# Kernel tuning notes

Hardware: AMD Instinct MI355X
Metric: run time of the kernel (lower is better)

## Reference

```python
import jax, jax.numpy as jnp
import numpy as np

N_NODES = 50000
N_EDGES = 800000
D_IN = 96
D_OUT = 96


def setup_inputs() -> dict:
    key = jax.random.key(0)
    k1, k2, k3 = jax.random.split(key, 3)
    x = jax.random.normal(k1, (N_NODES, D_IN), dtype=jnp.float32)
    edge_index = jax.random.randint(k2, (2, N_EDGES), 0, N_NODES, dtype=jnp.int64)
    edge_weight = jnp.ones((N_EDGES,), dtype=jnp.float32)
    # Glorot-ish init for the linear weight, zero bias (as in PyG GCNConv)
    W = jax.random.normal(k3, (D_IN, D_OUT), dtype=jnp.float32) * (1.0 / np.sqrt(D_IN))
    b = jnp.zeros((D_OUT,), dtype=jnp.float32)
    return {"x": x, "edge_index": edge_index, "edge_weight": edge_weight, "W": W, "b": b}


def reference(x, edge_index, edge_weight, W, b):
    """PyG GCNConv: out = D^{-1/2} (A + I) D^{-1/2} (x @ W) + b."""
    N = x.shape[0]
    row, col = edge_index[0], edge_index[1]  # source -> target
    # add self loops with weight 1 (PyG default add_self_loops=True)
    loop = jnp.arange(N, dtype=edge_index.dtype)
    row = jnp.concatenate([row, loop])
    col = jnp.concatenate([col, loop])
    ew = jnp.concatenate([edge_weight, jnp.ones((N,), dtype=edge_weight.dtype)])
    # symmetric normalization based on (weighted) in-degree over col
    deg = jax.ops.segment_sum(ew, col, num_segments=N)  # [N]
    dinv = jnp.where(deg > 0, jax.lax.rsqrt(deg), 0.0)
    norm = dinv[row] * ew * dinv[col]  # [E+N]
    # linear transform first (small GEMM), then gather-scale-scatter over edges
    h = x @ W  # [N, D_OUT]
    msg = h[row] * norm[:, None]  # [E+N, D_OUT]
    out = jax.ops.segment_sum(msg, col, num_segments=N)  # [N, D_OUT]
    return out + b
```

## Files before the change

### kernel.cpp

```cpp
#include <hip/hip_runtime.h>

#define N_NODES 50000
#define N_EDGES 800000
#define D 96
#define NBKT 512
#define BNODES 98
#define BCAP 2304
#define PART_B 250
#define EPB 3200
#define EPT 13
#define CAP 48
#define NSLOT (BNODES * CAP)
#define GCAP 768
#define GEMM_B 782

typedef float vfloat4 __attribute__((ext_vector_type(4)));

__device__ __forceinline__ float bf_lo(unsigned u) { return __uint_as_float(u << 16); }
__device__ __forceinline__ float bf_hi(unsigned u) { return __uint_as_float(u & 0xFFFF0000u); }
__device__ __forceinline__ unsigned f2bf_bits(unsigned u) {
    return (u + 0x7FFFu + ((u >> 16) & 1u)) & 0xFFFF0000u;
}
__device__ __forceinline__ unsigned pack_bf2(float a, float b) {
    return (f2bf_bits(__float_as_uint(a)) >> 16) | f2bf_bits(__float_as_uint(b));
}

__device__ __forceinline__ int exscan256(int v, int* wsum) {
    int lane = threadIdx.x & 63;
    int wave = threadIdx.x >> 6;
    int incl = v;
#pragma unroll
    for (int off = 1; off < 64; off <<= 1) {
        int t = __shfl_up(incl, off);
        if (lane >= off) incl += t;
    }
    if (lane == 63) wsum[wave] = incl;
    __syncthreads();
    int base = 0;
#pragma unroll
    for (int wv = 0; wv < 3; ++wv) base += (wv < wave) ? wsum[wv] : 0;
    return base + incl - v;
}

__global__ __launch_bounds__(256) void k_partgemm(
    const int* __restrict__ row, const int* __restrict__ col,
    const float* __restrict__ ew, const float* __restrict__ x,
    const float* __restrict__ W, int* __restrict__ bkt_cnt,
    uint2* __restrict__ bktbuf, unsigned short* __restrict__ hb) {
    __shared__ int sh[2 * NBKT];
    int tid = threadIdx.x;
    int bid = blockIdx.x;

    if (bid < PART_B) {
        int* hist = sh;
        int* cur = sh + NBKT;
        hist[tid] = 0;
        hist[tid + 256] = 0;
        __syncthreads();
        int e0 = bid * EPB;
        int myc[EPT];
#pragma unroll
        for (int k = 0; k < EPT; ++k) {
            int i = tid + 256 * k;
            myc[k] = (i < EPB) ? col[e0 + i] : -1;
        }
#pragma unroll
        for (int k = 0; k < EPT; ++k)
            if (myc[k] >= 0) atomicAdd(&hist[myc[k] / BNODES], 1);
        __syncthreads();
        {
            int h0 = hist[tid], h1 = hist[tid + 256];
            cur[tid] = h0 ? atomicAdd(&bkt_cnt[tid], h0) : 0;
            cur[tid + 256] = h1 ? atomicAdd(&bkt_cnt[tid + 256], h1) : 0;
        }
        __syncthreads();
#pragma unroll
        for (int k = 0; k < EPT; ++k) {
            int i = tid + 256 * k;
            if (myc[k] >= 0) {
                int e = e0 + i;
                int c = myc[k];
                int b = c / BNODES;
                int p = atomicAdd(&cur[b], 1);
                if (p < BCAP)
                    bktbuf[(size_t)b * BCAP + p] =
                        make_uint2((unsigned)row[e] | ((unsigned)(c - b * BNODES) << 16),
                                   __float_as_uint(ew[e]));
            }
        }
    } else {
        int g = bid - PART_B;
        int lane = tid & 63;
        int j0 = __builtin_amdgcn_readfirstlane((tid >> 6) * 24);
        int n = g * 64 + lane;
        bool act = (n < N_NODES);
        const float* xr = x + (size_t)(act ? n : 0) * D;

        float acc[24] = {};
        for (int k4 = 0; k4 < D / 4; ++k4) {
            float4 xv = *(const float4*)&xr[k4 * 4];
#pragma unroll
            for (int kk = 0; kk < 4; ++kk) {
                float xs = (kk == 0) ? xv.x : (kk == 1) ? xv.y
                         : (kk == 2) ? xv.z : xv.w;
                const float* Wr = W + (k4 * 4 + kk) * D + j0;
#pragma unroll
                for (int jj = 0; jj < 24; ++jj)
                    acc[jj] += xs * Wr[jj];
            }
        }
        if (act) {
            unsigned short* hp = hb + (size_t)n * D + j0;
            uint4 u0, u1, u2;
            u0.x = pack_bf2(acc[0], acc[1]);   u0.y = pack_bf2(acc[2], acc[3]);
            u0.z = pack_bf2(acc[4], acc[5]);   u0.w = pack_bf2(acc[6], acc[7]);
            u1.x = pack_bf2(acc[8], acc[9]);   u1.y = pack_bf2(acc[10], acc[11]);
            u1.z = pack_bf2(acc[12], acc[13]); u1.w = pack_bf2(acc[14], acc[15]);
            u2.x = pack_bf2(acc[16], acc[17]); u2.y = pack_bf2(acc[18], acc[19]);
            u2.z = pack_bf2(acc[20], acc[21]); u2.w = pack_bf2(acc[22], acc[23]);
            *(uint4*)(hp) = u0;
            *(uint4*)(hp + 8) = u1;
            *(uint4*)(hp + 16) = u2;
        }
    }
}

__global__ __launch_bounds__(256) void k_bin(const int* __restrict__ bkt_cnt,
                                             const uint2* __restrict__ bktbuf,
                                             unsigned* __restrict__ recs,
                                             int* __restrict__ rowptr,
                                             float* __restrict__ dinv) {
    __shared__ int wsum1[4];
    __shared__ int wsum2[4];
    __shared__ int sbkt[NBKT];
    __shared__ int lcnt[BNODES];
    __shared__ int loff[256];
    __shared__ unsigned lslot[NSLOT];
    int tid = threadIdx.x;
    int b = blockIdx.x;

    int c0 = min(bkt_cnt[2 * tid], BCAP);
    int c1 = min(bkt_cnt[2 * tid + 1], BCAP);
    int ps = exscan256(c0 + c1, wsum1);
    sbkt[2 * tid] = ps;
    sbkt[2 * tid + 1] = ps + c0;
    if (tid < BNODES) lcnt[tid] = 0;
    __syncthreads();
    int gbase = sbkt[b];
    int ne = min(bkt_cnt[b], BCAP);

    for (int i = tid; i < ne; i += 256) {
        uint2 r = bktbuf[(size_t)b * BCAP + i];
        int lc = (int)(r.x >> 16);
        int p = atomicAdd(&lcnt[lc], 1);
        if (p < CAP) lslot[lc * CAP + p] = f2bf_bits(r.y) | (r.x & 0xFFFFu);
    }
    __syncthreads();

    int myv = (tid < BNODES) ? min(lcnt[tid], CAP) : 0;
    int ex2 = exscan256(myv, wsum2);
    loff[tid] = ex2;
    __syncthreads();

    for (int i = tid; i < NSLOT; i += 256) {
        int ln = i / CAP, s = i % CAP;
        if (s < min(lcnt[ln], CAP))
            recs[gbase + loff[ln] + s] = lslot[i];
    }
    int base = b * BNODES;
    if (tid < BNODES) {
        int n = base + tid;
        if (n <= N_NODES) rowptr[n] = gbase + loff[tid];
        if (n < N_NODES) {
            int cn = min(lcnt[tid], CAP);
            float d = 1.0f;
            for (int k = 0; k < cn; ++k) d += bf_hi(lslot[tid * CAP + k]);
            dinv[n] = rsqrtf(d);
        }
    }
}

__global__ __launch_bounds__(192) void k_gather(const int* __restrict__ rowptr,
                                                const unsigned* __restrict__ recs,
                                                const unsigned short* __restrict__ hb,
                                                const float* __restrict__ dinv,
                                                const float* __restrict__ bias,
                                                float* __restrict__ out) {
    __shared__ uint2 sed[GCAP];
    __shared__ int sptr[17];
    __shared__ unsigned char perm[16];
    int tid = threadIdx.x;
    int nb = blockIdx.x * 16;

    if (tid < 17) sptr[tid] = rowptr[nb + tid];
    __syncthreads();
    if (tid < 16) {
        int dmy = sptr[tid + 1] - sptr[tid];
        int rank = 0;
#pragma unroll
        for (int jn = 0; jn < 16; ++jn) {
            int dj = sptr[jn + 1] - sptr[jn];
            rank += (dj > dmy) || (dj == dmy && jn < tid);
        }
        perm[rank] = (unsigned char)tid;
    }
    int e0 = sptr[0];
    int stage = sptr[16] - e0;
    for (int i = tid; i < stage; i += 192) {
        unsigned r = recs[e0 + i];
        int src = (int)(r & 0xFFFFu);
        sed[i] = make_uint2((unsigned)src,
                            __float_as_uint(bf_hi(r) * dinv[src]));
    }
    __syncthreads();

    int pl = perm[tid / 12];
    int jq = tid % 12;
    int n = nb + pl;
    int j = jq * 8;

    float di = dinv[n];
    uint4 sv = *(const uint4*)(hb + (size_t)n * D + j);
    float acc[8];
    acc[0] = bf_lo(sv.x) * di; acc[1] = bf_hi(sv.x) * di;
    acc[2] = bf_lo(sv.y) * di; acc[3] = bf_hi(sv.y) * di;
    acc[4] = bf_lo(sv.z) * di; acc[5] = bf_hi(sv.z) * di;
    acc[6] = bf_lo(sv.w) * di; acc[7] = bf_hi(sv.w) * di;

    int ls = sptr[pl] - e0;
    int le = sptr[pl + 1] - e0;
    int idx = ls;
    for (; idx + 4 <= le; idx += 4) {
        uint2 e0r = sed[idx], e1r = sed[idx + 1];
        uint2 e2r = sed[idx + 2], e3r = sed[idx + 3];
        uint4 v0 = *(const uint4*)(hb + (size_t)e0r.x * D + j);
        uint4 v1 = *(const uint4*)(hb + (size_t)e1r.x * D + j);
        uint4 v2 = *(const uint4*)(hb + (size_t)e2r.x * D + j);
        uint4 v3 = *(const uint4*)(hb + (size_t)e3r.x * D + j);
        float w0 = __uint_as_float(e0r.y), w1 = __uint_as_float(e1r.y);
        float w2 = __uint_as_float(e2r.y), w3 = __uint_as_float(e3r.y);
        acc[0] += w0 * bf_lo(v0.x); acc[1] += w0 * bf_hi(v0.x);
        acc[2] += w0 * bf_lo(v0.y); acc[3] += w0 * bf_hi(v0.y);
        acc[4] += w0 * bf_lo(v0.z); acc[5] += w0 * bf_hi(v0.z);
        acc[6] += w0 * bf_lo(v0.w); acc[7] += w0 * bf_hi(v0.w);
        acc[0] += w1 * bf_lo(v1.x); acc[1] += w1 * bf_hi(v1.x);
        acc[2] += w1 * bf_lo(v1.y); acc[3] += w1 * bf_hi(v1.y);
        acc[4] += w1 * bf_lo(v1.z); acc[5] += w1 * bf_hi(v1.z);
        acc[6] += w1 * bf_lo(v1.w); acc[7] += w1 * bf_hi(v1.w);
        acc[0] += w2 * bf_lo(v2.x); acc[1] += w2 * bf_hi(v2.x);
        acc[2] += w2 * bf_lo(v2.y); acc[3] += w2 * bf_hi(v2.y);
        acc[4] += w2 * bf_lo(v2.z); acc[5] += w2 * bf_hi(v2.z);
        acc[6] += w2 * bf_lo(v2.w); acc[7] += w2 * bf_hi(v2.w);
        acc[0] += w3 * bf_lo(v3.x); acc[1] += w3 * bf_hi(v3.x);
        acc[2] += w3 * bf_lo(v3.y); acc[3] += w3 * bf_hi(v3.y);
        acc[4] += w3 * bf_lo(v3.z); acc[5] += w3 * bf_hi(v3.z);
        acc[6] += w3 * bf_lo(v3.w); acc[7] += w3 * bf_hi(v3.w);
    }
    for (; idx < le; ++idx) {
        uint2 er = sed[idx];
        uint4 v0 = *(const uint4*)(hb + (size_t)er.x * D + j);
        float w0 = __uint_as_float(er.y);
        acc[0] += w0 * bf_lo(v0.x); acc[1] += w0 * bf_hi(v0.x);
        acc[2] += w0 * bf_lo(v0.y); acc[3] += w0 * bf_hi(v0.y);
        acc[4] += w0 * bf_lo(v0.z); acc[5] += w0 * bf_hi(v0.z);
        acc[6] += w0 * bf_lo(v0.w); acc[7] += w0 * bf_hi(v0.w);
    }

    float4 b0 = *(const float4*)&bias[j];
    float4 b1 = *(const float4*)&bias[j + 4];
    vfloat4 o0, o1;
    o0.x = acc[0] * di + b0.x; o0.y = acc[1] * di + b0.y;
    o0.z = acc[2] * di + b0.z; o0.w = acc[3] * di + b0.w;
    o1.x = acc[4] * di + b1.x; o1.y = acc[5] * di + b1.y;
    o1.z = acc[6] * di + b1.z; o1.w = acc[7] * di + b1.w;
    __builtin_nontemporal_store(o0, (vfloat4*)&out[(size_t)n * D + j]);
    __builtin_nontemporal_store(o1, (vfloat4*)&out[(size_t)n * D + j + 4]);
}

extern "C" void kernel_launch(void* const* d_in, const int* in_sizes, int n_in,
                              void* d_out, int out_size, void* d_ws, size_t ws_size,
                              hipStream_t stream) {
    const float* x  = (const float*)d_in[0];
    const int*   ei = (const int*)d_in[1];
    const float* ew = (const float*)d_in[2];
    const float* W  = (const float*)d_in[3];
    const float* b  = (const float*)d_in[4];
    float* out = (float*)d_out;

    const int* row = ei;
    const int* col = ei + N_EDGES;

    char* p = (char*)d_ws;
    unsigned short* hb     = (unsigned short*)p;   p += (size_t)N_NODES * D * 2;
    uint2*          bktbuf = (uint2*)p;            p += (size_t)NBKT * BCAP * 8;
    unsigned*       recs   = (unsigned*)p;         p += (size_t)N_EDGES * 4;
    int*            rowptr = (int*)p;              p += (size_t)(N_NODES + 64) * 4;
    float*          dinv   = (float*)p;            p += (size_t)N_NODES * 4;
    int*            bkt_cnt= (int*)p;              p += (size_t)NBKT * 4;

    (void)hipMemsetAsync(bkt_cnt, 0, NBKT * sizeof(int), stream);
    k_partgemm<<<PART_B + GEMM_B, 256, 0, stream>>>(row, col, ew, x, W,
                                                    bkt_cnt, bktbuf, hb);
    k_bin   <<<NBKT, 256, 0, stream>>>(bkt_cnt, bktbuf, recs, rowptr, dinv);
    k_gather<<<(N_NODES + 15) / 16, 192, 0, stream>>>(rowptr, recs, hb, dinv, b, out);
}
```

Measured before the change: 144.5 us.

## Replace bucket-bin CSR build with direct per-node slot scatter via global atomics

Drops the two-level bucket partition and the k_bin kernel that built CSR rowptr and records. The first kernel now scatters each edge straight into a fixed-capacity per-node slot array using global atomics on the per-node count and weighted degree. The gather kernel reads the slots directly and computes the normalisation rsqrt on the fly. This removes one kernel launch and an intermediate pass over memory, at the cost of many contended global atomics, a wider memset, and slot reads that are padded up to CAP per node.

```diff
diff --git a/kernel.cpp b/kernel.cpp
--- a/kernel.cpp
+++ b/kernel.cpp
@@ -3,16 +3,13 @@
 #define N_NODES 50000
 #define N_EDGES 800000
 #define D 96
-#define NBKT 512
-#define BNODES 98
-#define BCAP 2304
-#define PART_B 250
+#define SLOT_B 250
 #define EPB 3200
 #define EPT 13
 #define CAP 48
-#define NSLOT (BNODES * CAP)
-#define GCAP 768
 #define GEMM_B 782
+#define GCAP (16 * CAP)
+#define GATHER_B (N_NODES / 16)
 
 typedef float vfloat4 __attribute__((ext_vector_type(4)));
 
@@ -25,71 +22,34 @@
     return (f2bf_bits(__float_as_uint(a)) >> 16) | f2bf_bits(__float_as_uint(b));
 }
 
-__device__ __forceinline__ int exscan256(int v, int* wsum) {
-    int lane = threadIdx.x & 63;
-    int wave = threadIdx.x >> 6;
-    int incl = v;
-#pragma unroll
-    for (int off = 1; off < 64; off <<= 1) {
-        int t = __shfl_up(incl, off);
-        if (lane >= off) incl += t;
-    }
-    if (lane == 63) wsum[wave] = incl;
-    __syncthreads();
-    int base = 0;
-#pragma unroll
-    for (int wv = 0; wv < 3; ++wv) base += (wv < wave) ? wsum[wv] : 0;
-    return base + incl - v;
-}
-
-__global__ __launch_bounds__(256) void k_partgemm(
+__global__ __launch_bounds__(256) void k_slotgemm(
     const int* __restrict__ row, const int* __restrict__ col,
     const float* __restrict__ ew, const float* __restrict__ x,
-    const float* __restrict__ W, int* __restrict__ bkt_cnt,
-    uint2* __restrict__ bktbuf, unsigned short* __restrict__ hb) {
-    __shared__ int sh[2 * NBKT];
+    const float* __restrict__ W, int* __restrict__ cnt,
+    float* __restrict__ degw, unsigned* __restrict__ slot,
+    unsigned short* __restrict__ hb) {
     int tid = threadIdx.x;
     int bid = blockIdx.x;
 
-    if (bid < PART_B) {
-        int* hist = sh;
-        int* cur = sh + NBKT;
-        hist[tid] = 0;
-        hist[tid + 256] = 0;
-        __syncthreads();
+    if (bid < SLOT_B) {
         int e0 = bid * EPB;
-        int myc[EPT];
 #pragma unroll
         for (int k = 0; k < EPT; ++k) {
             int i = tid + 256 * k;
-            myc[k] = (i < EPB) ? col[e0 + i] : -1;
-        }
-#pragma unroll
-        for (int k = 0; k < EPT; ++k)
-            if (myc[k] >= 0) atomicAdd(&hist[myc[k] / BNODES], 1);
-        __syncthreads();
-        {
-            int h0 = hist[tid], h1 = hist[tid + 256];
-            cur[tid] = h0 ? atomicAdd(&bkt_cnt[tid], h0) : 0;
-            cur[tid + 256] = h1 ? atomicAdd(&bkt_cnt[tid + 256], h1) : 0;
-        }
-        __syncthreads();
-#pragma unroll
-        for (int k = 0; k < EPT; ++k) {
-            int i = tid + 256 * k;
-            if (myc[k] >= 0) {
+            if (i < EPB) {
                 int e = e0 + i;
-                int c = myc[k];
-                int b = c / BNODES;
-                int p = atomicAdd(&cur[b], 1);
-                if (p < BCAP)
-                    bktbuf[(size_t)b * BCAP + p] =
-                        make_uint2((unsigned)row[e] | ((unsigned)(c - b * BNODES) << 16),
-                                   __float_as_uint(ew[e]));
+                int c = col[e];
+                int r = row[e];
+                float w = ew[e];
+                atomicAdd(&degw[c], w);
+                int p = atomicAdd(&cnt[c], 1);
+                if (p < CAP)
+                    slot[(size_t)c * CAP + p] =
+                        f2bf_bits(__float_as_uint(w)) | (unsigned)r;
             }
         }
     } else {
-        int g = bid - PART_B;
+        int g = bid - SLOT_B;
         int lane = tid & 63;
         int j0 = __builtin_amdgcn_readfirstlane((tid >> 6) * 24);
         int n = g * 64 + lane;
@@ -125,92 +85,41 @@
     }
 }
 
-__global__ __launch_bounds__(256) void k_bin(const int* __restrict__ bkt_cnt,
-                                             const uint2* __restrict__ bktbuf,
-                                             unsigned* __restrict__ recs,
-                                             int* __restrict__ rowptr,
-                                             float* __restrict__ dinv) {
-    __shared__ int wsum1[4];
-    __shared__ int wsum2[4];
-    __shared__ int sbkt[NBKT];
-    __shared__ int lcnt[BNODES];
-    __shared__ int loff[256];
-    __shared__ unsigned lslot[NSLOT];
-    int tid = threadIdx.x;
-    int b = blockIdx.x;
-
-    int c0 = min(bkt_cnt[2 * tid], BCAP);
-    int c1 = min(bkt_cnt[2 * tid + 1], BCAP);
-    int ps = exscan256(c0 + c1, wsum1);
-    sbkt[2 * tid] = ps;
-    sbkt[2 * tid + 1] = ps + c0;
-    if (tid < BNODES) lcnt[tid] = 0;
-    __syncthreads();
-    int gbase = sbkt[b];
-    int ne = min(bkt_cnt[b], BCAP);
-
-    for (int i = tid; i < ne; i += 256) {
-        uint2 r = bktbuf[(size_t)b * BCAP + i];
-        int lc = (int)(r.x >> 16);
-        int p = atomicAdd(&lcnt[lc], 1);
-        if (p < CAP) lslot[lc * CAP + p] = f2bf_bits(r.y) | (r.x & 0xFFFFu);
-    }
-    __syncthreads();
-
-    int myv = (tid < BNODES) ? min(lcnt[tid], CAP) : 0;
-    int ex2 = exscan256(myv, wsum2);
-    loff[tid] = ex2;
-    __syncthreads();
-
-    for (int i = tid; i < NSLOT; i += 256) {
-        int ln = i / CAP, s = i % CAP;
-        if (s < min(lcnt[ln], CAP))
-            recs[gbase + loff[ln] + s] = lslot[i];
-    }
-    int base = b * BNODES;
-    if (tid < BNODES) {
-        int n = base + tid;
-        if (n <= N_NODES) rowptr[n] = gbase + loff[tid];
-        if (n < N_NODES) {
-            int cn = min(lcnt[tid], CAP);
-            float d = 1.0f;
-            for (int k = 0; k < cn; ++k) d += bf_hi(lslot[tid * CAP + k]);
-            dinv[n] = rsqrtf(d);
-        }
-    }
-}
-
-__global__ __launch_bounds__(192) void k_gather(const int* __restrict__ rowptr,
-                                                const unsigned* __restrict__ recs,
-                                                const unsigned short* __restrict__ hb,
-                                                const float* __restrict__ dinv,
-                                                const float* __restrict__ bias,
-                                                float* __restrict__ out) {
+__global__ __launch_bounds__(192) void k_gather(
+    const int* __restrict__ cnt, const float* __restrict__ degw,
+    const unsigned* __restrict__ slot, const unsigned short* __restrict__ hb,
+    const float* __restrict__ bias, float* __restrict__ out) {
     __shared__ uint2 sed[GCAP];
-    __shared__ int sptr[17];
+    __shared__ int scnt[16];
+    __shared__ float sdi[16];
     __shared__ unsigned char perm[16];
     int tid = threadIdx.x;
     int nb = blockIdx.x * 16;
 
-    if (tid < 17) sptr[tid] = rowptr[nb + tid];
+    if (tid < 16) {
+        int n = nb + tid;
+        scnt[tid] = min(cnt[n], CAP);
+        sdi[tid] = rsqrtf(1.0f + degw[n]);
+    }
     __syncthreads();
     if (tid < 16) {
-        int dmy = sptr[tid + 1] - sptr[tid];
+        int dmy = scnt[tid];
         int rank = 0;
 #pragma unroll
         for (int jn = 0; jn < 16; ++jn) {
-            int dj = sptr[jn + 1] - sptr[jn];
+            int dj = scnt[jn];
             rank += (dj > dmy) || (dj == dmy && jn < tid);
         }
         perm[rank] = (unsigned char)tid;
     }
-    int e0 = sptr[0];
-    int stage = sptr[16] - e0;
-    for (int i = tid; i < stage; i += 192) {
-        unsigned r = recs[e0 + i];
-        int src = (int)(r & 0xFFFFu);
-        sed[i] = make_uint2((unsigned)src,
-                            __float_as_uint(bf_hi(r) * dinv[src]));
+    for (int i = tid; i < GCAP; i += 192) {
+        int ln = i / CAP, s = i - ln * CAP;
+        if (s < scnt[ln]) {
+            unsigned r = slot[(size_t)(nb + ln) * CAP + s];
+            int src = (int)(r & 0xFFFFu);
+            sed[i] = make_uint2((unsigned)src,
+                __float_as_uint(bf_hi(r) * rsqrtf(1.0f + degw[src])));
+        }
     }
     __syncthreads();
 
@@ -219,7 +128,7 @@
     int n = nb + pl;
     int j = jq * 8;
 
-    float di = dinv[n];
+    float di = sdi[pl];
     uint4 sv = *(const uint4*)(hb + (size_t)n * D + j);
     float acc[8];
     acc[0] = bf_lo(sv.x) * di; acc[1] = bf_hi(sv.x) * di;
@@ -227,8 +136,8 @@
     acc[4] = bf_lo(sv.z) * di; acc[5] = bf_hi(sv.z) * di;
     acc[6] = bf_lo(sv.w) * di; acc[7] = bf_hi(sv.w) * di;
 
-    int ls = sptr[pl] - e0;
-    int le = sptr[pl + 1] - e0;
+    int ls = pl * CAP;
+    int le = ls + scnt[pl];
     int idx = ls;
     for (; idx + 4 <= le; idx += 4) {
         uint2 e0r = sed[idx], e1r = sed[idx + 1];
@@ -291,16 +200,13 @@
     const int* col = ei + N_EDGES;
 
     char* p = (char*)d_ws;
-    unsigned short* hb     = (unsigned short*)p;   p += (size_t)N_NODES * D * 2;
-    uint2*          bktbuf = (uint2*)p;            p += (size_t)NBKT * BCAP * 8;
-    unsigned*       recs   = (unsigned*)p;         p += (size_t)N_EDGES * 4;
-    int*            rowptr = (int*)p;              p += (size_t)(N_NODES + 64) * 4;
-    float*          dinv   = (float*)p;            p += (size_t)N_NODES * 4;
-    int*            bkt_cnt= (int*)p;              p += (size_t)NBKT * 4;
-
-    (void)hipMemsetAsync(bkt_cnt, 0, NBKT * sizeof(int), stream);
-    k_partgemm<<<PART_B + GEMM_B, 256, 0, stream>>>(row, col, ew, x, W,
-                                                    bkt_cnt, bktbuf, hb);
-    k_bin   <<<NBKT, 256, 0, stream>>>(bkt_cnt, bktbuf, recs, rowptr, dinv);
-    k_gather<<<(N_NODES + 15) / 16, 192, 0, stream>>>(rowptr, recs, hb, dinv, b, out);
-}
+    unsigned short* hb   = (unsigned short*)p;  p += (size_t)N_NODES * D * 2;
+    unsigned*       slot = (unsigned*)p;        p += (size_t)N_NODES * CAP * 4;
+    int*            cnt  = (int*)p;             p += (size_t)N_NODES * 4;
+    float*          degw = (float*)p;           p += (size_t)N_NODES * 4;
+
+    (void)hipMemsetAsync(cnt, 0, 2 * (size_t)N_NODES * sizeof(int), stream);
+    k_slotgemm<<<SLOT_B + GEMM_B, 256, 0, stream>>>(row, col, ew, x, W,
+                                                    cnt, degw, slot, hb);
+    k_gather<<<GATHER_B, 192, 0, stream>>>(cnt, degw, slot, hb, b, out);
+}
```

Measured after the change: 183.3 us. 1.27x slower.

## Fuse GEMM with binning kernel and widen gather tiles to 21 nodes

Applied to the files above, without the earlier changes.

The dense x@W GEMM blocks move out of the partition kernel and into the binning kernel, so the GEMM overlaps with binning instead of with partitioning. The partition kernel now runs on its own with 250 blocks. The gather kernel handles 21 nodes per block with 256 threads instead of 16 nodes with 192, which fills more lanes and adds a guard for inactive lanes. This rebalances work across stages, but the bin blocks now use a lot of LDS, and sharing a launch with GEMM blocks may limit occupancy.

```diff
diff --git a/kernel.cpp b/kernel.cpp
--- a/kernel.cpp
+++ b/kernel.cpp
@@ -11,8 +11,10 @@
 #define EPT 13
 #define CAP 48
 #define NSLOT (BNODES * CAP)
-#define GCAP 768
 #define GEMM_B 782
+#define NTILE 21
+#define GCAP (NTILE * CAP)
+#define GATHER_B ((N_NODES + NTILE - 1) / NTILE)
 
 typedef float vfloat4 __attribute__((ext_vector_type(4)));
 
@@ -42,54 +44,107 @@
     return base + incl - v;
 }
 
-__global__ __launch_bounds__(256) void k_partgemm(
-    const int* __restrict__ row, const int* __restrict__ col,
-    const float* __restrict__ ew, const float* __restrict__ x,
-    const float* __restrict__ W, int* __restrict__ bkt_cnt,
-    uint2* __restrict__ bktbuf, unsigned short* __restrict__ hb) {
-    __shared__ int sh[2 * NBKT];
+__global__ __launch_bounds__(256) void k_part(const int* __restrict__ row,
+                                              const int* __restrict__ col,
+                                              const float* __restrict__ ew,
+                                              int* __restrict__ bkt_cnt,
+                                              uint2* __restrict__ bktbuf) {
+    __shared__ int hist[NBKT];
+    __shared__ int cur[NBKT];
+    int tid = threadIdx.x;
+    hist[tid] = 0;
+    hist[tid + 256] = 0;
+    __syncthreads();
+    int e0 = blockIdx.x * EPB;
+    int myc[EPT];
+#pragma unroll
+    for (int k = 0; k < EPT; ++k) {
+        int i = tid + 256 * k;
+        myc[k] = (i < EPB) ? col[e0 + i] : -1;
+    }
+#pragma unroll
+    for (int k = 0; k < EPT; ++k)
+        if (myc[k] >= 0) atomicAdd(&hist[myc[k] / BNODES], 1);
+    __syncthreads();
+    {
+        int h0 = hist[tid], h1 = hist[tid + 256];
+        cur[tid] = h0 ? atomicAdd(&bkt_cnt[tid], h0) : 0;
+        cur[tid + 256] = h1 ? atomicAdd(&bkt_cnt[tid + 256], h1) : 0;
+    }
+    __syncthreads();
+#pragma unroll
+    for (int k = 0; k < EPT; ++k) {
+        int i = tid + 256 * k;
+        if (myc[k] >= 0) {
+            int e = e0 + i;
+            int c = myc[k];
+            int b = c / BNODES;
+            int p = atomicAdd(&cur[b], 1);
+            if (p < BCAP)
+                bktbuf[(size_t)b * BCAP + p] =
+                    make_uint2((unsigned)row[e] | ((unsigned)(c - b * BNODES) << 16),
+                               __float_as_uint(ew[e]));
+        }
+    }
+}
+
+__global__ __launch_bounds__(256) void k_bingemm(
+    const int* __restrict__ bkt_cnt, const uint2* __restrict__ bktbuf,
+    const float* __restrict__ x, const float* __restrict__ W,
+    unsigned* __restrict__ recs, int* __restrict__ rowptr,
+    float* __restrict__ dinv, unsigned short* __restrict__ hb) {
+    __shared__ int wsum1[4];
+    __shared__ int wsum2[4];
+    __shared__ int sbkt[NBKT];
+    __shared__ int lcnt[BNODES];
+    __shared__ int loff[256];
+    __shared__ unsigned lslot[NSLOT];
     int tid = threadIdx.x;
     int bid = blockIdx.x;
 
-    if (bid < PART_B) {
-        int* hist = sh;
-        int* cur = sh + NBKT;
-        hist[tid] = 0;
-        hist[tid + 256] = 0;
+    if (bid < NBKT) {
+        int b = bid;
+        int c0 = min(bkt_cnt[2 * tid], BCAP);
+        int c1 = min(bkt_cnt[2 * tid + 1], BCAP);
+        int ps = exscan256(c0 + c1, wsum1);
+        sbkt[2 * tid] = ps;
+        sbkt[2 * tid + 1] = ps + c0;
+        if (tid < BNODES) lcnt[tid] = 0;
         __syncthreads();
-        int e0 = bid * EPB;
-        int myc[EPT];
-#pragma unroll
-        for (int k = 0; k < EPT; ++k) {
-            int i = tid + 256 * k;
-            myc[k] = (i < EPB) ? col[e0 + i] : -1;
-        }
-#pragma unroll
-        for (int k = 0; k < EPT; ++k)
-            if (myc[k] >= 0) atomicAdd(&hist[myc[k] / BNODES], 1);
+        int gbase = sbkt[b];
+        int ne = min(bkt_cnt[b], BCAP);
+
+        for (int i = tid; i < ne; i += 256) {
+            uint2 r = bktbuf[(size_t)b * BCAP + i];
+            int lc = (int)(r.x >> 16);
+            int p = atomicAdd(&lcnt[lc], 1);
+            if (p < CAP) lslot[lc * CAP + p] = f2bf_bits(r.y) | (r.x & 0xFFFFu);
+        }
         __syncthreads();
-        {
-            int h0 = hist[tid], h1 = hist[tid + 256];
-            cur[tid] = h0 ? atomicAdd(&bkt_cnt[tid], h0) : 0;
-            cur[tid + 256] = h1 ? atomicAdd(&bkt_cnt[tid + 256], h1) : 0;
-        }
+
+        int myv = (tid < BNODES) ? min(lcnt[tid], CAP) : 0;
+        int ex2 = exscan256(myv, wsum2);
+        loff[tid] = ex2;
         __syncthreads();
-#pragma unroll
-        for (int k = 0; k < EPT; ++k) {
-            int i = tid + 256 * k;
-            if (myc[k] >= 0) {
-                int e = e0 + i;
-                int c = myc[k];
-                int b = c / BNODES;
-                int p = atomicAdd(&cur[b], 1);
-                if (p < BCAP)
-                    bktbuf[(size_t)b * BCAP + p] =
-                        make_uint2((unsigned)row[e] | ((unsigned)(c - b * BNODES) << 16),
-                                   __float_as_uint(ew[e]));
+
+        for (int i = tid; i < NSLOT; i += 256) {
+            int ln = i / CAP, s = i % CAP;
+            if (s < min(lcnt[ln], CAP))
+                recs[gbase + loff[ln] + s] = lslot[i];
+        }
+        int base = b * BNODES;
+        if (tid < BNODES) {
+            int n = base + tid;
+            if (n <= N_NODES) rowptr[n] = gbase + loff[tid];
+            if (n < N_NODES) {
+                int cn = min(lcnt[tid], CAP);
+                float d = 1.0f;
+                for (int k = 0; k < cn; ++k) d += bf_hi(lslot[tid * CAP + k]);
+                dinv[n] = rsqrtf(d);
             }
         }
     } else {
-        int g = bid - PART_B;
+        int g = bid - NBKT;
         int lane = tid & 63;
         int j0 = __builtin_amdgcn_readfirstlane((tid >> 6) * 24);
         int n = g * 64 + lane;
@@ -125,88 +180,33 @@
     }
 }
 
-__global__ __launch_bounds__(256) void k_bin(const int* __restrict__ bkt_cnt,
-                                             const uint2* __restrict__ bktbuf,
-                                             unsigned* __restrict__ recs,
-                                             int* __restrict__ rowptr,
-                                             float* __restrict__ dinv) {
-    __shared__ int wsum1[4];
-    __shared__ int wsum2[4];
-    __shared__ int sbkt[NBKT];
-    __shared__ int lcnt[BNODES];
-    __shared__ int loff[256];
-    __shared__ unsigned lslot[NSLOT];
-    int tid = threadIdx.x;
-    int b = blockIdx.x;
-
-    int c0 = min(bkt_cnt[2 * tid], BCAP);
-    int c1 = min(bkt_cnt[2 * tid + 1], BCAP);
-    int ps = exscan256(c0 + c1, wsum1);
-    sbkt[2 * tid] = ps;
-    sbkt[2 * tid + 1] = ps + c0;
-    if (tid < BNODES) lcnt[tid] = 0;
-    __syncthreads();
-    int gbase = sbkt[b];
-    int ne = min(bkt_cnt[b], BCAP);
-
-    for (int i = tid; i < ne; i += 256) {
-        uint2 r = bktbuf[(size_t)b * BCAP + i];
-        int lc = (int)(r.x >> 16);
-        int p = atomicAdd(&lcnt[lc], 1);
-        if (p < CAP) lslot[lc * CAP + p] = f2bf_bits(r.y) | (r.x & 0xFFFFu);
-    }
-    __syncthreads();
-
-    int myv = (tid < BNODES) ? min(lcnt[tid], CAP) : 0;
-    int ex2 = exscan256(myv, wsum2);
-    loff[tid] = ex2;
-    __syncthreads();
-
-    for (int i = tid; i < NSLOT; i += 256) {
-        int ln = i / CAP, s = i % CAP;
-        if (s < min(lcnt[ln], CAP))
-            recs[gbase + loff[ln] + s] = lslot[i];
-    }
-    int base = b * BNODES;
-    if (tid < BNODES) {
-        int n = base + tid;
-        if (n <= N_NODES) rowptr[n] = gbase + loff[tid];
-        if (n < N_NODES) {
-            int cn = min(lcnt[tid], CAP);
-            float d = 1.0f;
-            for (int k = 0; k < cn; ++k) d += bf_hi(lslot[tid * CAP + k]);
-            dinv[n] = rsqrtf(d);
-        }
-    }
-}
-
-__global__ __launch_bounds__(192) void k_gather(const int* __restrict__ rowptr,
+__global__ __launch_bounds__(256) void k_gather(const int* __restrict__ rowptr,
                                                 const unsigned* __restrict__ recs,
                                                 const unsigned short* __restrict__ hb,
                                                 const float* __restrict__ dinv,
                                                 const float* __restrict__ bias,
                                                 float* __restrict__ out) {
     __shared__ uint2 sed[GCAP];
-    __shared__ int sptr[17];
-    __shared__ unsigned char perm[16];
+    __shared__ int sptr[NTILE + 1];
+    __shared__ unsigned char perm[NTILE];
     int tid = threadIdx.x;
-    int nb = blockIdx.x * 16;
-
-    if (tid < 17) sptr[tid] = rowptr[nb + tid];
-    __syncthreads();
-    if (tid < 16) {
+    int nb = blockIdx.x * NTILE;
+
+    if (tid <= NTILE) sptr[tid] = rowptr[min(nb + tid, N_NODES)];
+    __syncthreads();
+    if (tid < NTILE) {
         int dmy = sptr[tid + 1] - sptr[tid];
         int rank = 0;
 #pragma unroll
-        for (int jn = 0; jn < 16; ++jn) {
+        for (int jn = 0; jn < NTILE; ++jn) {
             int dj = sptr[jn + 1] - sptr[jn];
             rank += (dj > dmy) || (dj == dmy && jn < tid);
         }
         perm[rank] = (unsigned char)tid;
     }
     int e0 = sptr[0];
-    int stage = sptr[16] - e0;
-    for (int i = tid; i < stage; i += 192) {
+    int stage = sptr[NTILE] - e0;
+    for (int i = tid; i < stage; i += 256) {
         unsigned r = recs[e0 + i];
         int src = (int)(r & 0xFFFFu);
         sed[i] = make_uint2((unsigned)src,
@@ -214,21 +214,25 @@
     }
     __syncthreads();
 
-    int pl = perm[tid / 12];
+    int lg = tid / 12;
     int jq = tid % 12;
+    int pl = (lg < NTILE) ? perm[lg] : 0;
     int n = nb + pl;
+    bool act = (lg < NTILE) && (n < N_NODES);
     int j = jq * 8;
 
-    float di = dinv[n];
-    uint4 sv = *(const uint4*)(hb + (size_t)n * D + j);
-    float acc[8];
-    acc[0] = bf_lo(sv.x) * di; acc[1] = bf_hi(sv.x) * di;
-    acc[2] = bf_lo(sv.y) * di; acc[3] = bf_hi(sv.y) * di;
-    acc[4] = bf_lo(sv.z) * di; acc[5] = bf_hi(sv.z) * di;
-    acc[6] = bf_lo(sv.w) * di; acc[7] = bf_hi(sv.w) * di;
-
-    int ls = sptr[pl] - e0;
-    int le = sptr[pl + 1] - e0;
+    float di = act ? dinv[n] : 0.f;
+    float acc[8] = {};
+    if (act) {
+        uint4 sv = *(const uint4*)(hb + (size_t)n * D + j);
+        acc[0] = bf_lo(sv.x) * di; acc[1] = bf_hi(sv.x) * di;
+        acc[2] = bf_lo(sv.y) * di; acc[3] = bf_hi(sv.y) * di;
+        acc[4] = bf_lo(sv.z) * di; acc[5] = bf_hi(sv.z) * di;
+        acc[6] = bf_lo(sv.w) * di; acc[7] = bf_hi(sv.w) * di;
+    }
+
+    int ls = act ? (sptr[pl] - e0) : 0;
+    int le = act ? (sptr[pl + 1] - e0) : 0;
     int idx = ls;
     for (; idx + 4 <= le; idx += 4) {
         uint2 e0r = sed[idx], e1r = sed[idx + 1];
@@ -266,15 +270,17 @@
         acc[6] += w0 * bf_lo(v0.w); acc[7] += w0 * bf_hi(v0.w);
     }
 
-    float4 b0 = *(const float4*)&bias[j];
-    float4 b1 = *(const float4*)&bias[j + 4];
-    vfloat4 o0, o1;
-    o0.x = acc[0] * di + b0.x; o0.y = acc[1] * di + b0.y;
-    o0.z = acc[2] * di + b0.z; o0.w = acc[3] * di + b0.w;
-    o1.x = acc[4] * di + b1.x; o1.y = acc[5] * di + b1.y;
-    o1.z = acc[6] * di + b1.z; o1.w = acc[7] * di + b1.w;
-    __builtin_nontemporal_store(o0, (vfloat4*)&out[(size_t)n * D + j]);
-    __builtin_nontemporal_store(o1, (vfloat4*)&out[(size_t)n * D + j + 4]);
+    if (act) {
+        float4 b0 = *(const float4*)&bias[j];
+        float4 b1 = *(const float4*)&bias[j + 4];
+        vfloat4 o0, o1;
+        o0.x = acc[0] * di + b0.x; o0.y = acc[1] * di + b0.y;
+        o0.z = acc[2] * di + b0.z; o0.w = acc[3] * di + b0.w;
+        o1.x = acc[4] * di + b1.x; o1.y = acc[5] * di + b1.y;
+        o1.z = acc[6] * di + b1.z; o1.w = acc[7] * di + b1.w;
+        __builtin_nontemporal_store(o0, (vfloat4*)&out[(size_t)n * D + j]);
+        __builtin_nontemporal_store(o1, (vfloat4*)&out[(size_t)n * D + j + 4]);
+    }
 }
 
 extern "C" void kernel_launch(void* const* d_in, const int* in_sizes, int n_in,
@@ -299,8 +305,8 @@
     int*            bkt_cnt= (int*)p;              p += (size_t)NBKT * 4;
 
     (void)hipMemsetAsync(bkt_cnt, 0, NBKT * sizeof(int), stream);
-    k_partgemm<<<PART_B + GEMM_B, 256, 0, stream>>>(row, col, ew, x, W,
-                                                    bkt_cnt, bktbuf, hb);
-    k_bin   <<<NBKT, 256, 0, stream>>>(bkt_cnt, bktbuf, recs, rowptr, dinv);
-    k_gather<<<(N_NODES + 15) / 16, 192, 0, stream>>>(rowptr, recs, hb, dinv, b, out);
-}
+    k_part   <<<PART_B, 256, 0, stream>>>(row, col, ew, bkt_cnt, bktbuf);
+    k_bingemm<<<NBKT + GEMM_B, 256, 0, stream>>>(bkt_cnt, bktbuf, x, W,
+                                                 recs, rowptr, dinv, hb);
+    k_gather <<<GATHER_B, 256, 0, stream>>>(rowptr, recs, hb, dinv, b, out);
+}
```

New measurement: 141.7 us. No clear change (-1.9%).
